# Kernel optimization log

Hardware: AMD Instinct MI355X
Metric: run time of the kernel (lower is better)

## Reference

```python
import jax, jax.numpy as jnp
import numpy as np

B, S, D, H, O = 32, 2048, 512, 512, 512


def setup_inputs() -> dict:
    key = jax.random.key(0)
    ks = jax.random.split(key, 10)
    def w(k, shape, fan_in):
        return (jax.random.uniform(k, shape, dtype=jnp.float32) * 2.0 - 1.0) / np.float32(np.sqrt(fan_in))
    return {
        "x": jax.random.normal(ks[0], (B, S, D), dtype=jnp.float32),
        "timespans": jax.random.uniform(ks[1], (B, S, 1), dtype=jnp.float32),
        "Wx_lstm": w(ks[2], (D, 4 * H), D),
        "Wh_lstm": w(ks[3], (H, 4 * H), H),
        "b_lstm": jnp.zeros((4 * H,), dtype=jnp.float32),
        "Wx_ode": w(ks[4], (D, H), D),
        "Wh_ode": w(ks[5], (H, H), H),
        "b_ode": jnp.zeros((H,), dtype=jnp.float32),
        "Wfc": w(ks[6], (H, O), H),
        "bfc": jnp.zeros((O,), dtype=jnp.float32),
    }


def reference(x, timespans, Wx_lstm, Wh_lstm, b_lstm, Wx_ode, Wh_ode, b_ode, Wfc, bfc):
    b, s, d = x.shape
    h_dim = Wh_ode.shape[0]
    # Precompute input projections for all timesteps (hoisted out of the scan).
    xz_lstm = jnp.einsum('bsd,dk->bsk', x, Wx_lstm) + b_lstm   # (B,S,4H)
    xz_ode = jnp.einsum('bsd,dh->bsh', x, Wx_ode) + b_ode      # (B,S,H)
    ts = timespans[..., 0]                                      # (B,S), matches ts.squeeze()

    def step(carry, inp):
        h, c = carry
        zl, zo, t = inp                      # (B,4H), (B,H), (B,)
        # LSTM memory update (mixed-memory part)
        z = zl + h @ Wh_lstm
        i, f, g, o = jnp.split(z, 4, axis=-1)
        c_new = jax.nn.sigmoid(f) * c + jax.nn.sigmoid(i) * jnp.tanh(g)
        h_mem = jax.nn.sigmoid(o) * jnp.tanh(c_new)
        # Heun (RK2) ODE step: dh/dt = tanh(Wx x + Wh h + b)
        def f_ode(hh):
            return jnp.tanh(zo + hh @ Wh_ode)
        tcol = t[:, None]
        k1 = f_ode(h_mem)
        k2 = f_ode(h_mem + tcol * k1)
        h_new = h_mem + 0.5 * tcol * (k1 + k2)
        return (h_new, c_new), h_new

    carry0 = (jnp.zeros((b, h_dim), x.dtype), jnp.zeros((b, h_dim), x.dtype))
    xs = (jnp.swapaxes(xz_lstm, 0, 1), jnp.swapaxes(xz_ode, 0, 1), ts.T)
    (h_last, c_last), hs = jax.lax.scan(step, carry0, xs)       # hs: (S,B,H)
    outputs = jnp.einsum('sbh,ho->sbo', hs, Wfc) + bfc
    outputs = jnp.swapaxes(outputs, 0, 1)                       # (B,S,O)
    return outputs, h_last, c_last
```

## Files before the change

### kernel.cpp

```cpp
#include <hip/hip_runtime.h>

typedef unsigned short u16;
typedef unsigned int u32;
typedef unsigned long long u64;
typedef __attribute__((ext_vector_type(4))) float f32x4;
typedef __attribute__((ext_vector_type(8))) short bf16x8;
typedef __attribute__((ext_vector_type(4))) u16 u16x4;
typedef __attribute__((ext_vector_type(8))) u16 u16x8;
typedef __attribute__((ext_vector_type(4))) u32 u32x4;

#define AGENT_SCOPE __HIP_MEMORY_SCOPE_AGENT

__device__ __forceinline__ u64 lda64(const u64* p) {
  return __hip_atomic_load((u64*)p, __ATOMIC_RELAXED, AGENT_SCOPE);
}
__device__ __forceinline__ int loadai(const int* p) {
  return __hip_atomic_load((int*)p, __ATOMIC_RELAXED, AGENT_SCOPE);
}
__device__ __forceinline__ void sta32(u32* p, u32 v) {
  __hip_atomic_store(p, v, __ATOMIC_RELAXED, AGENT_SCOPE);
}

__device__ __forceinline__ u16 f2bf(float f) {
  u32 u = __builtin_bit_cast(u32, f);
  u = (u + 0x7FFFu + ((u >> 16) & 1u)) >> 16;
  return (u16)u;
}
__device__ __forceinline__ float b2f(u16 h) {
  return __builtin_bit_cast(float, ((u32)h) << 16);
}
__device__ __forceinline__ float sigf(float x) { return 1.0f / (1.0f + __expf(-x)); }
__device__ __forceinline__ float tanh_(float x) { return 2.0f / (1.0f + __expf(-2.0f * x)) - 1.0f; }

__global__ __launch_bounds__(256) void cvt_bf16_vec(
    const float* __restrict__ in, u16* __restrict__ out, int n4)
{
  int i = blockIdx.x * blockDim.x + threadIdx.x;
  const int stride = gridDim.x * blockDim.x;
  for (; i < n4; i += stride) {
    f32x4 v = ((const f32x4*)in)[i];
    u16x4 o;
    #pragma unroll
    for (int e = 0; e < 4; ++e) o[e] = f2bf(v[e]);
    ((u16x4*)out)[i] = o;
  }
}

__global__ __launch_bounds__(256) void transpose_f32_bf16(
    const float* __restrict__ in, u16* __restrict__ out, int R, int C)
{
  __shared__ float t[32][33];
  const int tx = threadIdx.x & 31, ty = threadIdx.x >> 5;
  const int bx = blockIdx.x * 32, by = blockIdx.y * 32;
  #pragma unroll
  for (int i = 0; i < 4; ++i)
    t[ty + i * 8][tx] = in[(long)(by + ty + i * 8) * C + bx + tx];
  __syncthreads();
  #pragma unroll
  for (int i = 0; i < 4; ++i)
    out[(long)(bx + ty + i * 8) * R + by + tx] = f2bf(t[tx][ty + i * 8]);
}

template <bool BF16_OUT>
__global__ __launch_bounds__(256, 2) void gemm_bt(
    const u16* __restrict__ A, const u16* __restrict__ Bt,
    const float* __restrict__ bias, void* __restrict__ Cv,
    int M, int N, int K)
{
  __shared__ u16 As[128 * 64];
  __shared__ u16 Bs[128 * 64];
  const int tid = threadIdx.x;
  const int lane = tid & 63;
  const int wv = tid >> 6;
  const int wm = wv >> 1, wn = wv & 1;
  const long row0 = (long)blockIdx.x * 128;
  const long col0 = (long)blockIdx.y * 128;
  const int lr8 = lane >> 3, lc8 = lane & 7;
  const int fr = lane & 15, fk = (lane >> 4) * 8;
  f32x4 acc[4][4] = {};

  for (int kt = 0; kt < K; kt += 64) {
    __syncthreads();
    #pragma unroll
    for (int ch = 0; ch < 4; ++ch) {
      const int r = wv * 32 + ch * 8;
      const u16* gA = A + (row0 + r + lr8) * (long)K + kt + lc8 * 8;
      __builtin_amdgcn_global_load_lds(
          (const __attribute__((address_space(1))) u32*)gA,
          (__attribute__((address_space(3))) u32*)&As[r * 64], 16, 0, 0);
      const u16* gB = Bt + (col0 + r + lr8) * (long)K + kt + lc8 * 8;
      __builtin_amdgcn_global_load_lds(
          (const __attribute__((address_space(1))) u32*)gB,
          (__attribute__((address_space(3))) u32*)&Bs[r * 64], 16, 0, 0);
    }
    __syncthreads();
    #pragma unroll
    for (int kk = 0; kk < 2; ++kk) {
      bf16x8 af[4], bfv[4];
      #pragma unroll
      for (int m = 0; m < 4; ++m)
        af[m] = *(const bf16x8*)&As[(wm * 64 + m * 16 + fr) * 64 + kk * 32 + fk];
      #pragma unroll
      for (int n = 0; n < 4; ++n)
        bfv[n] = *(const bf16x8*)&Bs[(wn * 64 + n * 16 + fr) * 64 + kk * 32 + fk];
      #pragma unroll
      for (int m = 0; m < 4; ++m)
        #pragma unroll
        for (int n = 0; n < 4; ++n)
          acc[m][n] = __builtin_amdgcn_mfma_f32_16x16x32_bf16(af[m], bfv[n], acc[m][n], 0, 0, 0);
    }
  }

  const int orow = (lane >> 4) * 4, ocol = lane & 15;
  #pragma unroll
  for (int m = 0; m < 4; ++m) {
    #pragma unroll
    for (int n = 0; n < 4; ++n) {
      const long cb = col0 + wn * 64 + n * 16 + ocol;
      const float bv = bias[cb];
      #pragma unroll
      for (int r = 0; r < 4; ++r) {
        const long rr = row0 + wm * 64 + m * 16 + orow + r;
        const float v = acc[m][n][r] + bv;
        if (BF16_OUT) ((u16*)Cv)[rr * (long)N + cb] = f2bf(v);
        else          ((float*)Cv)[rr * (long)N + cb] = v;
      }
    }
  }
}

#define SS 2048
#define FAROFF 16384

__device__ __forceinline__ bool ge4(u32x4 v, u32 t) {
  return ((v[0] >> 16) >= t) & ((v[1] >> 16) >= t) &
         ((v[2] >> 16) >= t) & ((v[3] >> 16) >= t);
}
__device__ __forceinline__ bool ge2(u64 w, u32 t) {
  return ((((u32)(w >> 16)) & 0xffffu) >= t) & (((u32)(w >> 48)) >= t);
}

__device__ __forceinline__ void ld8_sc0(const u32* p, u32x4& a, u32x4& b) {
  asm volatile("global_load_dwordx4 %0, %2, off sc0\n\t"
               "global_load_dwordx4 %1, %3, off sc0\n\t"
               "s_waitcnt vmcnt(0)"
               : "=&v"(a), "=&v"(b) : "v"(p), "v"(p + 4));
}
__device__ __forceinline__ void ld8_sc1(const u32* p, u32x4& a, u32x4& b) {
  asm volatile("global_load_dwordx4 %0, %2, off sc1\n\t"
               "global_load_dwordx4 %1, %3, off sc1\n\t"
               "s_waitcnt vmcnt(0)"
               : "=&v"(a), "=&v"(b) : "v"(p), "v"(p + 4));
}

__device__ __forceinline__ void pollfar(const u32* pf, u32 tag, u32x4& a, u32x4& b) {
  const u64* q = (const u64*)pf;
  u64 w0 = lda64(q), w1 = lda64(q + 1), w2 = lda64(q + 2), w3 = lda64(q + 3);
  int tries = 0;
  while (!(ge2(w0, tag) & ge2(w1, tag) & ge2(w2, tag) & ge2(w3, tag))) {
    if (++tries > 2) __builtin_amdgcn_s_sleep(1);
    w0 = lda64(q); w1 = lda64(q + 1); w2 = lda64(q + 2); w3 = lda64(q + 3);
  }
  a[0] = (u32)w0; a[1] = (u32)(w0 >> 32); a[2] = (u32)w1; a[3] = (u32)(w1 >> 32);
  b[0] = (u32)w2; b[1] = (u32)(w2 >> 32); b[2] = (u32)w3; b[3] = (u32)(w3 >> 32);
}

__device__ __forceinline__ void poll8(const u32* pn, u32 tag, int lvl, int* lvlsh,
                                      u32x4& a, u32x4& b) {
  if (lvl == 0) {
    int tries = 0;
    for (;;) {
      ld8_sc0(pn, a, b);
      if (ge4(a, tag) && ge4(b, tag)) return;
      if (++tries > 8000) { *lvlsh = 1; lvl = 1; break; }
      if (tries > 32) __builtin_amdgcn_s_sleep(1);
    }
  }
  if (lvl == 1) {
    int tries = 0;
    for (;;) {
      ld8_sc1(pn, a, b);
      if (ge4(a, tag) && ge4(b, tag)) return;
      if (++tries > 8000) { *lvlsh = 2; break; }
      if (tries > 32) __builtin_amdgcn_s_sleep(1);
    }
  }
  pollfar(pn + FAROFF, tag, a, b);
}

__global__ __launch_bounds__(256, 1) void scan_kernel(
    const u16* __restrict__ XZL, const float* __restrict__ XZO,
    const float* __restrict__ TS,
    const u16* __restrict__ WhlT, const u16* __restrict__ WhoT,
    u32* Ht, u32* HMt, u32* Ut,
    u16* __restrict__ HS,
    float* __restrict__ out_h, float* __restrict__ out_c,
    int* chk)
{
  const int tid = threadIdx.x;
  const int lane = tid & 63;
  const int wv = tid >> 6;
  const int fr = lane & 15;
  const int hi = lane >> 4;

  __shared__ u16 whl_l[4][16][512];
  __shared__ u16 who_l[16][512];
  __shared__ u16 stage_l[4][512];
  __shared__ u16 xcl[256];
  __shared__ int lvl_sh;

  if (tid == 0) {
    u32 xcc;
    asm volatile("s_getreg_b32 %0, hwreg(HW_REG_XCC_ID)" : "=s"(xcc));
    sta32((u32*)&chk[blockIdx.x], (xcc & 7u) + 1u);
    lvl_sh = 0;
  }
  {
    int v;
    do { v = loadai(&chk[tid]); } while (v == 0);
    xcl[tid] = (u16)(v - 1);
  }
  __syncthreads();

  int g, w;
  bool far_grp;
  {
    int cnt[8] = {0, 0, 0, 0, 0, 0, 0, 0};
    const int my = (int)xcl[blockIdx.x];
    int rank = 0;
    for (int bi = 0; bi < 256; ++bi) {
      const int e = (int)xcl[bi];
      ++cnt[e];
      rank += (e == my && bi < (int)blockIdx.x) ? 1 : 0;
    }
    bool ok = true;
    #pragma unroll
    for (int e = 0; e < 8; ++e) ok = ok && (cnt[e] == 32);
    if (ok) { g = my; w = rank; far_grp = false; }
    else    { g = (int)(blockIdx.x & 7); w = (int)(blockIdx.x >> 3); far_grp = true; }
  }
  const int j0 = w * 16;
  const int b = g * 4 + wv;

  {
    const int g4 = wv;
    #pragma unroll
    for (int ks = 0; ks < 16; ++ks)
      *(u16x8*)&whl_l[g4][ks][lane * 8] =
        *(const u16x8*)&WhlT[(size_t)(g4 * 512 + j0 + fr) * 512 + ks * 32 + (lane >> 4) * 8];
    for (int ks = wv; ks < 16; ks += 4)
      *(u16x8*)&who_l[ks][lane * 8] =
        *(const u16x8*)&WhoT[(size_t)(j0 + fr) * 512 + ks * 32 + (lane >> 4) * 8];
  }
  __syncthreads();

  const int kc8 = hi * 8;
  u32* const Hb  = Ht  + g * 2048 + wv * 512;
  u32* const HMb = HMt + g * 2048 + wv * 512;
  u32* const Ub  = Ut  + g * 2048 + wv * 512;

  float zb_c[4], zo_c, t_c;
  {
    const u16* p = XZL + ((size_t)b * SS + 0) * 2048 + j0 + fr;
    zb_c[0] = b2f(p[0]); zb_c[1] = b2f(p[512]);
    zb_c[2] = b2f(p[1024]); zb_c[3] = b2f(p[1536]);
    zo_c = XZO[((size_t)b * SS + 0) * 512 + j0 + fr];
    t_c  = TS[(size_t)b * SS + 0];
  }

  float c_r = 0.0f;
  u32x4 pa, pb;
  u32* pend_p = nullptr;
  u32  pend_w = 0;
  float hn_pend = 0.0f;

  for (int s = 0; s < SS; ++s) {
    const u32 tagv = (u32)(s + 1);
    int lvl = far_grp ? 2 : *(volatile int*)&lvl_sh;

    if (s == 0) {
      u16x8 z8 = {0, 0, 0, 0, 0, 0, 0, 0};
      *(u16x8*)&stage_l[wv][lane * 8] = z8;
    } else {
      if (hi == 0 && lvl >= 2 && pend_p) { sta32(pend_p, pend_w); pend_p = nullptr; }
      poll8(Hb + lane * 8, (u32)s, lvl, &lvl_sh, pa, pb);
      u16x8 hv;
      #pragma unroll
      for (int i = 0; i < 4; ++i) {
        hv[i] = (u16)(pa[i] & 0xffffu);
        hv[4 + i] = (u16)(pb[i] & 0xffffu);
      }
      *(u16x8*)&stage_l[wv][lane * 8] = hv;
      if (hi == 0) {
        if (pend_p) { sta32(pend_p, pend_w); pend_p = nullptr; }
        HS[((size_t)b * SS + (s - 1)) * 512 + j0 + fr] = f2bf(hn_pend);
      }
    }

    f32x4 az0a = {}, az0b = {}, az1a = {}, az1b = {};
    f32x4 az2a = {}, az2b = {}, az3a = {}, az3b = {};
    #pragma unroll
    for (int ks = 0; ks < 8; ++ks) {
      bf16x8 afa = *(const bf16x8*)&stage_l[wv][ks * 32 + kc8];
      bf16x8 afb = *(const bf16x8*)&stage_l[wv][(ks + 8) * 32 + kc8];
      az0a = __builtin_amdgcn_mfma_f32_16x16x32_bf16(afa, *(const bf16x8*)&whl_l[0][ks][lane * 8], az0a, 0, 0, 0);
      az0b = __builtin_amdgcn_mfma_f32_16x16x32_bf16(afb, *(const bf16x8*)&whl_l[0][ks + 8][lane * 8], az0b, 0, 0, 0);
      az1a = __builtin_amdgcn_mfma_f32_16x16x32_bf16(afa, *(const bf16x8*)&whl_l[1][ks][lane * 8], az1a, 0, 0, 0);
      az1b = __builtin_amdgcn_mfma_f32_16x16x32_bf16(afb, *(const bf16x8*)&whl_l[1][ks + 8][lane * 8], az1b, 0, 0, 0);
      az2a = __builtin_amdgcn_mfma_f32_16x16x32_bf16(afa, *(const bf16x8*)&whl_l[2][ks][lane * 8], az2a, 0, 0, 0);
      az2b = __builtin_amdgcn_mfma_f32_16x16x32_bf16(afb, *(const bf16x8*)&whl_l[2][ks + 8][lane * 8], az2b, 0, 0, 0);
      az3a = __builtin_amdgcn_mfma_f32_16x16x32_bf16(afa, *(const bf16x8*)&whl_l[3][ks][lane * 8], az3a, 0, 0, 0);
      az3b = __builtin_amdgcn_mfma_f32_16x16x32_bf16(afb, *(const bf16x8*)&whl_l[3][ks + 8][lane * 8], az3b, 0, 0, 0);
    }

    const float zi = az0a[0] + az0b[0] + zb_c[0];
    const float zf = az1a[0] + az1b[0] + zb_c[1];
    const float zg = az2a[0] + az2b[0] + zb_c[2];
    const float zo = az3a[0] + az3b[0] + zb_c[3];
    const float cn = sigf(zf) * c_r + sigf(zi) * tanh_(zg);
    const float hm = sigf(zo) * tanh_(cn);
    c_r = cn;
    if (hi == 0) {
      const u32 wd = (tagv << 16) | (u32)f2bf(hm);
      if (!far_grp)
        asm volatile("global_store_dword %0, %1, off sc1" :: "v"(&HMb[j0 + fr]), "v"(wd) : "memory");
      pend_p = &HMb[j0 + fr] + FAROFF; pend_w = wd;
    }

    lvl = far_grp ? 2 : *(volatile int*)&lvl_sh;
    if (hi == 0 && lvl >= 2 && pend_p) { sta32(pend_p, pend_w); pend_p = nullptr; }
    poll8(HMb + lane * 8, tagv, lvl, &lvl_sh, pa, pb);

    const int sn = (s + 1 < SS) ? s + 1 : s;
    float zb_n[4], zo_n, t_n;
    {
      const u16* p = XZL + ((size_t)b * SS + sn) * 2048 + j0 + fr;
      zb_n[0] = b2f(p[0]); zb_n[1] = b2f(p[512]);
      zb_n[2] = b2f(p[1024]); zb_n[3] = b2f(p[1536]);
      zo_n = XZO[((size_t)b * SS + sn) * 512 + j0 + fr];
      t_n  = TS[(size_t)b * SS + sn];
    }
    if (hi == 0 && pend_p) { sta32(pend_p, pend_w); pend_p = nullptr; }
    {
      u16x8 hv;
      #pragma unroll
      for (int i = 0; i < 4; ++i) {
        hv[i] = (u16)(pa[i] & 0xffffu);
        hv[4 + i] = (u16)(pb[i] & 0xffffu);
      }
      *(u16x8*)&stage_l[wv][lane * 8] = hv;
    }
    f32x4 aka = {}, akb = {};
    #pragma unroll
    for (int ks = 0; ks < 8; ++ks) {
      bf16x8 afa = *(const bf16x8*)&stage_l[wv][ks * 32 + kc8];
      bf16x8 afb = *(const bf16x8*)&stage_l[wv][(ks + 8) * 32 + kc8];
      aka = __builtin_amdgcn_mfma_f32_16x16x32_bf16(afa, *(const bf16x8*)&who_l[ks][lane * 8], aka, 0, 0, 0);
      akb = __builtin_amdgcn_mfma_f32_16x16x32_bf16(afb, *(const bf16x8*)&who_l[ks + 8][lane * 8], akb, 0, 0, 0);
    }
    const float k1 = tanh_(zo_c + aka[0] + akb[0]);
    const float uu = hm + t_c * k1;
    if (hi == 0) {
      const u32 wd = (tagv << 16) | (u32)f2bf(uu);
      if (!far_grp)
        asm volatile("global_store_dword %0, %1, off sc1" :: "v"(&Ub[j0 + fr]), "v"(wd) : "memory");
      pend_p = &Ub[j0 + fr] + FAROFF; pend_w = wd;
    }

    lvl = far_grp ? 2 : *(volatile int*)&lvl_sh;
    if (hi == 0 && lvl >= 2 && pend_p) { sta32(pend_p, pend_w); pend_p = nullptr; }
    poll8(Ub + lane * 8, tagv, lvl, &lvl_sh, pa, pb);
    if (hi == 0 && pend_p) { sta32(pend_p, pend_w); pend_p = nullptr; }
    {
      u16x8 hv;
      #pragma unroll
      for (int i = 0; i < 4; ++i) {
        hv[i] = (u16)(pa[i] & 0xffffu);
        hv[4 + i] = (u16)(pb[i] & 0xffffu);
      }
      *(u16x8*)&stage_l[wv][lane * 8] = hv;
    }
    f32x4 a2a = {}, a2b = {};
    #pragma unroll
    for (int ks = 0; ks < 8; ++ks) {
      bf16x8 afa = *(const bf16x8*)&stage_l[wv][ks * 32 + kc8];
      bf16x8 afb = *(const bf16x8*)&stage_l[wv][(ks + 8) * 32 + kc8];
      a2a = __builtin_amdgcn_mfma_f32_16x16x32_bf16(afa, *(const bf16x8*)&who_l[ks][lane * 8], a2a, 0, 0, 0);
      a2b = __builtin_amdgcn_mfma_f32_16x16x32_bf16(afb, *(const bf16x8*)&who_l[ks + 8][lane * 8], a2b, 0, 0, 0);
    }
    const float k2 = tanh_(zo_c + a2a[0] + a2b[0]);
    const float hn = hm + 0.5f * t_c * (k1 + k2);
    if (hi == 0) {
      const u32 wd = (tagv << 16) | (u32)f2bf(hn);
      if (!far_grp)
        asm volatile("global_store_dword %0, %1, off sc1" :: "v"(&Hb[j0 + fr]), "v"(wd) : "memory");
      pend_p = &Hb[j0 + fr] + FAROFF; pend_w = wd;
      hn_pend = hn;
    }

    #pragma unroll
    for (int i = 0; i < 4; ++i) zb_c[i] = zb_n[i];
    zo_c = zo_n; t_c = t_n;
  }

  if (hi == 0) {
    if (pend_p) sta32(pend_p, pend_w);
    HS[((size_t)b * SS + (SS - 1)) * 512 + j0 + fr] = f2bf(hn_pend);
    out_h[(size_t)b * 512 + j0 + fr] = hn_pend;
    out_c[(size_t)b * 512 + j0 + fr] = c_r;
  }
}

extern "C" void kernel_launch(void* const* d_in, const int* in_sizes, int n_in,
                              void* d_out, int out_size, void* d_ws, size_t ws_size,
                              hipStream_t stream)
{
  const long B = 32, S = 2048, O = 512;
  const long MS = B * S;

  const float* x   = (const float*)d_in[0];
  const float* ts  = (const float*)d_in[1];
  const float* Wxl = (const float*)d_in[2];
  const float* Whl = (const float*)d_in[3];
  const float* bl  = (const float*)d_in[4];
  const float* Wxo = (const float*)d_in[5];
  const float* Who = (const float*)d_in[6];
  const float* bo  = (const float*)d_in[7];
  const float* Wfc = (const float*)d_in[8];
  const float* bfc = (const float*)d_in[9];

  float* out = (float*)d_out;
  float* out_h = out + MS * O;
  float* out_c = out_h + B * 512;

  char* ws = (char*)d_ws;
  size_t off = 0;
  auto alloc = [&](size_t bytes) -> void* {
    void* p = ws + off;
    off += (bytes + 255) & ~(size_t)255;
    return p;
  };
  u16*   XZL  = (u16*)  alloc(MS * 2048 * 2);
  u16*   xb   = (u16*)  alloc(MS * 512 * 2);
  u16*   HS   = xb;
  u16*   WxlT = (u16*)  alloc(2048 * 512 * 2);
  u16*   WhlT = (u16*)  alloc(2048 * 512 * 2);
  u16*   WxoT = (u16*)  alloc(512 * 512 * 2);
  u16*   WhoT = (u16*)  alloc(512 * 512 * 2);
  u16*   WfcT = (u16*)  alloc(512 * 512 * 2);
  u32*   Ht   = (u32*)  alloc(2 * 8 * 2048 * 4);
  u32*   HMt  = (u32*)  alloc(2 * 8 * 2048 * 4);
  u32*   Ut   = (u32*)  alloc(2 * 8 * 2048 * 4);
  int*   chk  = (int*)  alloc(1024);

  float* XZO = out;

  if (off > ws_size) return;

  hipMemsetAsync(Ht, 0, 2 * 8 * 2048 * 4, stream);
  hipMemsetAsync(HMt, 0, 2 * 8 * 2048 * 4, stream);
  hipMemsetAsync(Ut, 0, 2 * 8 * 2048 * 4, stream);
  hipMemsetAsync(chk, 0, 1024, stream);

  cvt_bf16_vec<<<2048, 256, 0, stream>>>(x, xb, (int)(MS * 512 / 4));
  transpose_f32_bf16<<<dim3(64, 16), 256, 0, stream>>>(Wxl, WxlT, 512, 2048);
  transpose_f32_bf16<<<dim3(64, 16), 256, 0, stream>>>(Whl, WhlT, 512, 2048);
  transpose_f32_bf16<<<dim3(16, 16), 256, 0, stream>>>(Wxo, WxoT, 512, 512);
  transpose_f32_bf16<<<dim3(16, 16), 256, 0, stream>>>(Who, WhoT, 512, 512);
  transpose_f32_bf16<<<dim3(16, 16), 256, 0, stream>>>(Wfc, WfcT, 512, 512);

  gemm_bt<true ><<<dim3(512, 16), 256, 0, stream>>>(xb, WxlT, bl, XZL, (int)MS, 2048, 512);
  gemm_bt<false><<<dim3(512, 4), 256, 0, stream>>>(xb, WxoT, bo, XZO, (int)MS, 512, 512);

  {
    void* args[] = { (void*)&XZL, (void*)&XZO, (void*)&ts, (void*)&WhlT, (void*)&WhoT,
                     (void*)&Ht, (void*)&HMt, (void*)&Ut, (void*)&HS,
                     (void*)&out_h, (void*)&out_c, (void*)&chk };
    hipLaunchCooperativeKernel((void*)scan_kernel, dim3(256), dim3(256), args, 0, stream);
  }

  gemm_bt<false><<<dim3(512, 4), 256, 0, stream>>>(HS, WfcT, bfc, out, (int)MS, 512, 512);
}
```

Measured before the change: 13.77 ms.

## Drop far-mirror fallback stores and simplify the cross-block polling protocol

Removes the duplicate 'far' mirror buffer and the deferred pending-store path, so each step writes its tagged value once with an sc1 store instead of also writing a mirror copy. Polling now starts with sc0 loads and falls back to sc1 loads indefinitely, with a longer spin before sleeping. The next-step input prefetch moves to the top of the loop, ahead of the first matmul. This cuts store traffic and branching on the serial critical path. It risks lower robustness if XCC grouping fails, since the sc1 fallback must now carry all coherence.

After: 12.94 ms. -6.0%, faster.

```diff
diff --git a/kernel.cpp b/kernel.cpp
--- a/kernel.cpp
+++ b/kernel.cpp
@@ -11,9 +11,6 @@
 
 #define AGENT_SCOPE __HIP_MEMORY_SCOPE_AGENT
 
-__device__ __forceinline__ u64 lda64(const u64* p) {
-  return __hip_atomic_load((u64*)p, __ATOMIC_RELAXED, AGENT_SCOPE);
-}
 __device__ __forceinline__ int loadai(const int* p) {
   return __hip_atomic_load((int*)p, __ATOMIC_RELAXED, AGENT_SCOPE);
 }
@@ -130,14 +127,10 @@
 }
 
 #define SS 2048
-#define FAROFF 16384
 
 __device__ __forceinline__ bool ge4(u32x4 v, u32 t) {
   return ((v[0] >> 16) >= t) & ((v[1] >> 16) >= t) &
          ((v[2] >> 16) >= t) & ((v[3] >> 16) >= t);
-}
-__device__ __forceinline__ bool ge2(u64 w, u32 t) {
-  return ((((u32)(w >> 16)) & 0xffffu) >= t) & (((u32)(w >> 48)) >= t);
 }
 
 __device__ __forceinline__ void ld8_sc0(const u32* p, u32x4& a, u32x4& b) {
@@ -151,18 +144,6 @@
                "global_load_dwordx4 %1, %3, off sc1\n\t"
                "s_waitcnt vmcnt(0)"
                : "=&v"(a), "=&v"(b) : "v"(p), "v"(p + 4));
-}
-
-__device__ __forceinline__ void pollfar(const u32* pf, u32 tag, u32x4& a, u32x4& b) {
-  const u64* q = (const u64*)pf;
-  u64 w0 = lda64(q), w1 = lda64(q + 1), w2 = lda64(q + 2), w3 = lda64(q + 3);
-  int tries = 0;
-  while (!(ge2(w0, tag) & ge2(w1, tag) & ge2(w2, tag) & ge2(w3, tag))) {
-    if (++tries > 2) __builtin_amdgcn_s_sleep(1);
-    w0 = lda64(q); w1 = lda64(q + 1); w2 = lda64(q + 2); w3 = lda64(q + 3);
-  }
-  a[0] = (u32)w0; a[1] = (u32)(w0 >> 32); a[2] = (u32)w1; a[3] = (u32)(w1 >> 32);
-  b[0] = (u32)w2; b[1] = (u32)(w2 >> 32); b[2] = (u32)w3; b[3] = (u32)(w3 >> 32);
 }
 
 __device__ __forceinline__ void poll8(const u32* pn, u32 tag, int lvl, int* lvlsh,
@@ -172,20 +153,19 @@
     for (;;) {
       ld8_sc0(pn, a, b);
       if (ge4(a, tag) && ge4(b, tag)) return;
-      if (++tries > 8000) { *lvlsh = 1; lvl = 1; break; }
-      if (tries > 32) __builtin_amdgcn_s_sleep(1);
-    }
-  }
-  if (lvl == 1) {
-    int tries = 0;
-    for (;;) {
-      ld8_sc1(pn, a, b);
-      if (ge4(a, tag) && ge4(b, tag)) return;
-      if (++tries > 8000) { *lvlsh = 2; break; }
-      if (tries > 32) __builtin_amdgcn_s_sleep(1);
-    }
-  }
-  pollfar(pn + FAROFF, tag, a, b);
+      if (++tries > 8000) { *lvlsh = 1; break; }
+      if (tries > 256) __builtin_amdgcn_s_sleep(1);
+    }
+  }
+  for (;;) {
+    ld8_sc1(pn, a, b);
+    if (ge4(a, tag) && ge4(b, tag)) return;
+    __builtin_amdgcn_s_sleep(1);
+  }
+}
+
+__device__ __forceinline__ void stnear(u32* pn, u32 word) {
+  asm volatile("global_store_dword %0, %1, off sc1" :: "v"(pn), "v"(word) : "memory");
 }
 
 __global__ __launch_bounds__(256, 1) void scan_kernel(
@@ -223,7 +203,6 @@
   __syncthreads();
 
   int g, w;
-  bool far_grp;
   {
     int cnt[8] = {0, 0, 0, 0, 0, 0, 0, 0};
     const int my = (int)xcl[blockIdx.x];
@@ -236,8 +215,9 @@
     bool ok = true;
     #pragma unroll
     for (int e = 0; e < 8; ++e) ok = ok && (cnt[e] == 32);
-    if (ok) { g = my; w = rank; far_grp = false; }
-    else    { g = (int)(blockIdx.x & 7); w = (int)(blockIdx.x >> 3); far_grp = true; }
+    if (ok) { g = my; w = rank; }
+    else    { g = (int)(blockIdx.x & 7); w = (int)(blockIdx.x >> 3);
+              if (tid == 0) lvl_sh = 1; }
   }
   const int j0 = w * 16;
   const int b = g * 4 + wv;
@@ -270,19 +250,16 @@
 
   float c_r = 0.0f;
   u32x4 pa, pb;
-  u32* pend_p = nullptr;
-  u32  pend_w = 0;
   float hn_pend = 0.0f;
 
   for (int s = 0; s < SS; ++s) {
     const u32 tagv = (u32)(s + 1);
-    int lvl = far_grp ? 2 : *(volatile int*)&lvl_sh;
+    int lvl = *(volatile int*)&lvl_sh;
 
     if (s == 0) {
       u16x8 z8 = {0, 0, 0, 0, 0, 0, 0, 0};
       *(u16x8*)&stage_l[wv][lane * 8] = z8;
     } else {
-      if (hi == 0 && lvl >= 2 && pend_p) { sta32(pend_p, pend_w); pend_p = nullptr; }
       poll8(Hb + lane * 8, (u32)s, lvl, &lvl_sh, pa, pb);
       u16x8 hv;
       #pragma unroll
@@ -291,10 +268,17 @@
         hv[4 + i] = (u16)(pb[i] & 0xffffu);
       }
       *(u16x8*)&stage_l[wv][lane * 8] = hv;
-      if (hi == 0) {
-        if (pend_p) { sta32(pend_p, pend_w); pend_p = nullptr; }
+      if (hi == 0)
         HS[((size_t)b * SS + (s - 1)) * 512 + j0 + fr] = f2bf(hn_pend);
-      }
+    }
+    const int sn = (s + 1 < SS) ? s + 1 : s;
+    float zb_n[4], zo_n, t_n;
+    {
+      const u16* p = XZL + ((size_t)b * SS + sn) * 2048 + j0 + fr;
+      zb_n[0] = b2f(p[0]); zb_n[1] = b2f(p[512]);
+      zb_n[2] = b2f(p[1024]); zb_n[3] = b2f(p[1536]);
+      zo_n = XZO[((size_t)b * SS + sn) * 512 + j0 + fr];
+      t_n  = TS[(size_t)b * SS + sn];
     }
 
     f32x4 az0a = {}, az0b = {}, az1a = {}, az1b = {};
@@ -320,27 +304,11 @@
     const float cn = sigf(zf) * c_r + sigf(zi) * tanh_(zg);
     const float hm = sigf(zo) * tanh_(cn);
     c_r = cn;
-    if (hi == 0) {
-      const u32 wd = (tagv << 16) | (u32)f2bf(hm);
-      if (!far_grp)
-        asm volatile("global_store_dword %0, %1, off sc1" :: "v"(&HMb[j0 + fr]), "v"(wd) : "memory");
-      pend_p = &HMb[j0 + fr] + FAROFF; pend_w = wd;
-    }
-
-    lvl = far_grp ? 2 : *(volatile int*)&lvl_sh;
-    if (hi == 0 && lvl >= 2 && pend_p) { sta32(pend_p, pend_w); pend_p = nullptr; }
+    if (hi == 0)
+      stnear(&HMb[j0 + fr], (tagv << 16) | (u32)f2bf(hm));
+
+    lvl = *(volatile int*)&lvl_sh;
     poll8(HMb + lane * 8, tagv, lvl, &lvl_sh, pa, pb);
-
-    const int sn = (s + 1 < SS) ? s + 1 : s;
-    float zb_n[4], zo_n, t_n;
-    {
-      const u16* p = XZL + ((size_t)b * SS + sn) * 2048 + j0 + fr;
-      zb_n[0] = b2f(p[0]); zb_n[1] = b2f(p[512]);
-      zb_n[2] = b2f(p[1024]); zb_n[3] = b2f(p[1536]);
-      zo_n = XZO[((size_t)b * SS + sn) * 512 + j0 + fr];
-      t_n  = TS[(size_t)b * SS + sn];
-    }
-    if (hi == 0 && pend_p) { sta32(pend_p, pend_w); pend_p = nullptr; }
     {
       u16x8 hv;
       #pragma unroll
@@ -360,17 +328,11 @@
     }
     const float k1 = tanh_(zo_c + aka[0] + akb[0]);
     const float uu = hm + t_c * k1;
-    if (hi == 0) {
-      const u32 wd = (tagv << 16) | (u32)f2bf(uu);
-      if (!far_grp)
-        asm volatile("global_store_dword %0, %1, off sc1" :: "v"(&Ub[j0 + fr]), "v"(wd) : "memory");
-      pend_p = &Ub[j0 + fr] + FAROFF; pend_w = wd;
-    }
-
-    lvl = far_grp ? 2 : *(volatile int*)&lvl_sh;
-    if (hi == 0 && lvl >= 2 && pend_p) { sta32(pend_p, pend_w); pend_p = nullptr; }
+    if (hi == 0)
+      stnear(&Ub[j0 + fr], (tagv << 16) | (u32)f2bf(uu));
+
+    lvl = *(volatile int*)&lvl_sh;
     poll8(Ub + lane * 8, tagv, lvl, &lvl_sh, pa, pb);
-    if (hi == 0 && pend_p) { sta32(pend_p, pend_w); pend_p = nullptr; }
     {
       u16x8 hv;
       #pragma unroll
@@ -391,10 +353,7 @@
     const float k2 = tanh_(zo_c + a2a[0] + a2b[0]);
     const float hn = hm + 0.5f * t_c * (k1 + k2);
     if (hi == 0) {
-      const u32 wd = (tagv << 16) | (u32)f2bf(hn);
-      if (!far_grp)
-        asm volatile("global_store_dword %0, %1, off sc1" :: "v"(&Hb[j0 + fr]), "v"(wd) : "memory");
-      pend_p = &Hb[j0 + fr] + FAROFF; pend_w = wd;
+      stnear(&Hb[j0 + fr], (tagv << 16) | (u32)f2bf(hn));
       hn_pend = hn;
     }
 
@@ -404,7 +363,6 @@
   }
 
   if (hi == 0) {
-    if (pend_p) sta32(pend_p, pend_w);
     HS[((size_t)b * SS + (SS - 1)) * 512 + j0 + fr] = f2bf(hn_pend);
     out_h[(size_t)b * 512 + j0 + fr] = hn_pend;
     out_c[(size_t)b * 512 + j0 + fr] = c_r;
@@ -448,18 +406,18 @@
   u16*   WxoT = (u16*)  alloc(512 * 512 * 2);
   u16*   WhoT = (u16*)  alloc(512 * 512 * 2);
   u16*   WfcT = (u16*)  alloc(512 * 512 * 2);
-  u32*   Ht   = (u32*)  alloc(2 * 8 * 2048 * 4);
-  u32*   HMt  = (u32*)  alloc(2 * 8 * 2048 * 4);
-  u32*   Ut   = (u32*)  alloc(2 * 8 * 2048 * 4);
+  u32*   Ht   = (u32*)  alloc(8 * 2048 * 4);
+  u32*   HMt  = (u32*)  alloc(8 * 2048 * 4);
+  u32*   Ut   = (u32*)  alloc(8 * 2048 * 4);
   int*   chk  = (int*)  alloc(1024);
 
   float* XZO = out;
 
   if (off > ws_size) return;
 
-  hipMemsetAsync(Ht, 0, 2 * 8 * 2048 * 4, stream);
-  hipMemsetAsync(HMt, 0, 2 * 8 * 2048 * 4, stream);
-  hipMemsetAsync(Ut, 0, 2 * 8 * 2048 * 4, stream);
+  hipMemsetAsync(Ht, 0, 8 * 2048 * 4, stream);
+  hipMemsetAsync(HMt, 0, 8 * 2048 * 4, stream);
+  hipMemsetAsync(Ut, 0, 8 * 2048 * 4, stream);
   hipMemsetAsync(chk, 0, 1024, stream);
 
   cvt_bf16_vec<<<2048, 256, 0, stream>>>(x, xb, (int)(MS * 512 / 4));
```
